# Kernel optimization log

Hardware: AMD Instinct MI355X
Metric: run time of the kernel (lower is better)

## Reference

```python
import jax, jax.numpy as jnp
import numpy as np

B, S, H = 4, 8192, 768
NH, HD = 12, 64          # num_heads, head_size
M = 64                   # projection_dim = min(256, HD)
EPS = 1e-6

def setup_inputs() -> dict:
    key = jax.random.key(0)
    ks = jax.random.split(key, 10)
    scale_w = 0.02
    scale_p = 1.0 / np.sqrt(HD)
    return {
        'hidden_states': jax.random.normal(ks[0], (B, S, H), jnp.float32),
        'Wq': jax.random.normal(ks[1], (H, H), jnp.float32) * scale_w,
        'bq': jnp.zeros((H,), jnp.float32),
        'Wk': jax.random.normal(ks[2], (H, H), jnp.float32) * scale_w,
        'bk': jnp.zeros((H,), jnp.float32),
        'Wv': jax.random.normal(ks[3], (H, H), jnp.float32) * scale_w,
        'bv': jnp.zeros((H,), jnp.float32),
        'Wo': jax.random.normal(ks[4], (H, H), jnp.float32) * scale_w,
        'bo': jnp.zeros((H,), jnp.float32),
        'projection_matrix': jax.random.normal(ks[5], (NH, HD, M), jnp.float32) * scale_p,
    }

def reference(hidden_states, Wq, bq, Wk, bk, Wv, bv, Wo, bo, projection_matrix):
    b, s, h = hidden_states.shape
    def heads(x):  # [b,s,h] -> [b,nh,s,hd]
        return x.reshape(b, s, NH, HD).transpose(0, 2, 1, 3)
    q = heads(hidden_states @ Wq + bq)
    k = heads(hidden_states @ Wk + bk)
    v = heads(hidden_states @ Wv + bv)
    # random-feature projection + stabilized exp feature map
    qp = jnp.einsum('bhnd,hdm->bhnm', q, projection_matrix)
    kp = jnp.einsum('bhnd,hdm->bhnm', k, projection_matrix)
    qp = jnp.exp(qp - jnp.max(qp, axis=-1, keepdims=True))
    kp = jnp.exp(kp - jnp.max(kp, axis=-1, keepdims=True))
    # O(n) linear attention: kv summary [b,h,m,hd]
    kv = jnp.einsum('bhnm,bhnd->bhmd', kp, v)
    qkv = jnp.einsum('bhnm,bhmd->bhnd', qp, kv)
    k_sum = jnp.sum(kp, axis=2)                      # [b,h,m]
    normalizer = jnp.einsum('bhnm,bhm->bhn', qp, k_sum)[..., None]
    ctx = qkv / (normalizer + EPS)
    ctx = ctx.transpose(0, 2, 1, 3).reshape(b, s, NH * HD)
    return ctx @ Wo + bo
```

## Files before the change

### kernel.cpp

```cpp
#include <hip/hip_runtime.h>
#include <hip/hip_bf16.h>


#define S_    8192
#define H_    768
#define NH_   12
#define EPS_  1e-6f

typedef unsigned short U16;
typedef short bf16x8 __attribute__((ext_vector_type(8)));
typedef float f32x4  __attribute__((ext_vector_type(4)));

__device__ __forceinline__ U16 f2b(float x) {
  unsigned u = __float_as_uint(x);
  return (U16)((u + 0x7fffu + ((u >> 16) & 1u)) >> 16);
}
__device__ __forceinline__ float b2f(U16 h) {
  return __uint_as_float(((unsigned)h) << 16);
}
__device__ __forceinline__ void gl2lds16(const void* g, void* l) {
  __builtin_amdgcn_global_load_lds(
      (const __attribute__((address_space(1))) void*)g,
      (__attribute__((address_space(3))) void*)l, 16, 0, 0);
}

__global__ __launch_bounds__(256) void prologue(
    const float* __restrict__ hs, const float* __restrict__ Wq,
    const float* __restrict__ bq, const float* __restrict__ Wk,
    const float* __restrict__ bk, const float* __restrict__ Wv,
    const float* __restrict__ bv, const float* __restrict__ Wo,
    const float* __restrict__ P,
    U16* __restrict__ hs_hi, U16* __restrict__ WcatH, U16* __restrict__ WoTH,
    float* __restrict__ biasC, float* __restrict__ zbase) {
  __shared__ float sm[8192];
  const int bid = blockIdx.x, tid = threadIdx.x;
  if (bid < 960) {
    zbase[bid * 256 + tid] = 0.f;
    return;
  }
  if (bid < 25536) {
    int i = (bid - 960) * 256 + tid;
    float4 x = ((const float4*)hs)[i];
    ushort4 h;
    h.x = f2b(x.x); h.y = f2b(x.y); h.z = f2b(x.z); h.w = f2b(x.w);
    ((ushort4*)hs_hi)[i] = h;
    return;
  }
  if (bid < 25824) {
    int f = bid - 25536;
    int z = f / 144, rem = f - z * 144, h = rem / 12, kcB = rem - (rem / 12) * 12;
    float* Pl = sm;
    float* WL = sm + 4096;
    const float* W = z ? Wk : Wq;
    const float4* P4 = (const float4*)(P + (size_t)h * 4096);
#pragma unroll
    for (int p = 0; p < 4; ++p) ((float4*)Pl)[tid + p * 256] = P4[tid + p * 256];
#pragma unroll
    for (int p = 0; p < 4; ++p) {
      int idx = tid + p * 256;
      int kk = idx >> 4, d4 = (idx & 15) * 4;
      *(float4*)&WL[kk * 64 + d4] =
          *(const float4*)&W[(size_t)(kcB * 64 + kk) * H_ + h * 64 + d4];
    }
    __syncthreads();
    const int m = tid & 63, kg = tid >> 6;
    float acc[16] = {};
    for (int d = 0; d < 64; ++d) {
      float pv = Pl[d * 64 + m];
#pragma unroll
      for (int k2 = 0; k2 < 16; ++k2) acc[k2] += WL[(kg * 16 + k2) * 64 + d] * pv;
    }
    U16* dst = WcatH + (size_t)(z * 768 + h * 64 + m) * H_ + kcB * 64 + kg * 16;
#pragma unroll
    for (int k2 = 0; k2 < 16; k2 += 4) {
      ushort4 o;
      o.x = f2b(acc[k2]); o.y = f2b(acc[k2 + 1]);
      o.z = f2b(acc[k2 + 2]); o.w = f2b(acc[k2 + 3]);
      *(ushort4*)&dst[k2] = o;
    }
    if (kcB == 0 && tid < 64) {
      const float* bb = z ? bk : bq;
      float a2 = 0.f;
      for (int d = 0; d < 64; ++d) a2 += bb[h * 64 + d] * Pl[d * 64 + tid];
      biasC[z * 768 + h * 64 + tid] = a2;
    }
    return;
  }
  const int isWo = bid >= 25968;
  int v = bid - (isWo ? 25968 : 25824);
  int kb = v / 12, rb = v - kb * 12;
  const float* W = isWo ? Wo : Wv;
  float (*T)[68] = (float(*)[68])sm;
#pragma unroll
  for (int p = 0; p < 4; ++p) {
    int idx = tid + p * 256;
    int rr = idx >> 4, c4 = (idx & 15) * 4;
    float4 x = *(const float4*)&W[(size_t)(kb * 64 + rr) * H_ + rb * 64 + c4];
    T[rr][c4] = x.x; T[rr][c4 + 1] = x.y; T[rr][c4 + 2] = x.z; T[rr][c4 + 3] = x.w;
  }
  __syncthreads();
  U16* dst = isWo ? WoTH : WcatH;
  const int rbase = (isWo ? 0 : 1536) + rb * 64;
#pragma unroll
  for (int p = 0; p < 4; ++p) {
    int idx = tid + p * 256;
    int r2 = idx >> 4, c2 = (idx & 15) * 4;
    ushort4 o;
    o.x = f2b(T[c2 + 0][r2]); o.y = f2b(T[c2 + 1][r2]);
    o.z = f2b(T[c2 + 2][r2]); o.w = f2b(T[c2 + 3][r2]);
    *(ushort4*)&dst[(size_t)(rbase + r2) * H_ + kb * 64 + c2] = o;
  }
  if (!isWo && kb == 0 && rb == 0) {
#pragma unroll
    for (int p = 0; p < 3; ++p) biasC[1536 + tid + p * 256] = bv[tid + p * 256];
  }
}

__global__ __launch_bounds__(256, 2) void gemm_qkv(
    const U16* __restrict__ Ahi, const U16* __restrict__ Bhi,
    const float* __restrict__ bias,
    U16* __restrict__ qp, U16* __restrict__ kpT, U16* __restrict__ vT) {
  __shared__ __align__(16) U16 Us[32768];
  const int tid = threadIdx.x, w = tid >> 6, lane = tid & 63;
  const int quad = lane >> 4, l16 = lane & 15;
  const int b = blockIdx.x;
  const int mt = b & 255, nt0 = b >> 8;
  const int rowA0 = mt * 128;
  const int wm = w & 1, wn = w >> 1;
  const U16* srcA[4];
  int rowBl[4];
  unsigned ldsc[4];
  const int kch = ((lane & 7) ^ (lane >> 3)) * 8;
#pragma unroll
  for (int t = 0; t < 4; ++t) {
    int c = w * 4 + t;
    int row = c * 8 + (lane >> 3);
    srcA[t] = Ahi + (size_t)(rowA0 + row) * H_ + kch;
    rowBl[t] = row;
    ldsc[t] = (unsigned)c * 512;
  }
  auto stage = [&](int jn, int tn, int bi) {
    const int colB = (nt0 + 2 * jn) * 128;
    unsigned ub = (unsigned)bi * 16384u;
#pragma unroll
    for (int t = 0; t < 4; ++t) {
      gl2lds16(srcA[t] + tn * 64, &Us[ub + ldsc[t]]);
      gl2lds16(Bhi + (size_t)(colB + rowBl[t]) * H_ + tn * 64 + kch,
               &Us[ub + 8192u + ldsc[t]]);
    }
  };

  stage(0, 0, 0);
  for (int jj = 0; jj < 9; ++jj) {
    const int colB0 = (nt0 + 2 * jj) * 128;
    f32x4 acc[4][4] = {};
    for (int t = 0; t < 12; ++t) {
      const bool more = !(jj == 8 && t == 11);
      if (more) {
        if (t < 11) stage(jj, t + 1, (t + 1) & 1);
        else        stage(jj + 1, 0, 0);
        asm volatile("s_waitcnt vmcnt(8)" ::: "memory");
      } else {
        asm volatile("s_waitcnt vmcnt(0)" ::: "memory");
      }
      __builtin_amdgcn_sched_barrier(0);
      __builtin_amdgcn_s_barrier();
      __builtin_amdgcn_sched_barrier(0);
      const unsigned ab = (unsigned)(t & 1) * 16384u;
      bf16x8 ah[4][2], bh[4][2];
#pragma unroll
      for (int i = 0; i < 4; ++i)
#pragma unroll
        for (int ks = 0; ks < 2; ++ks)
          ah[i][ks] = *(const bf16x8*)&Us[ab +
              (unsigned)((wm * 64 + i * 16 + l16) * 64 +
                         (((ks * 4 + quad) ^ (l16 & 7)) * 8))];
#pragma unroll
      for (int j = 0; j < 4; ++j)
#pragma unroll
        for (int ks = 0; ks < 2; ++ks)
          bh[j][ks] = *(const bf16x8*)&Us[ab + 8192u +
              (unsigned)((wn * 64 + j * 16 + l16) * 64 +
                         (((ks * 4 + quad) ^ (l16 & 7)) * 8))];
      asm volatile("s_waitcnt lgkmcnt(0)" ::: "memory");
      __builtin_amdgcn_sched_barrier(0);
      __builtin_amdgcn_s_setprio(1);
#pragma unroll
      for (int ks = 0; ks < 2; ++ks)
#pragma unroll
        for (int j = 0; j < 4; ++j)
#pragma unroll
          for (int i = 0; i < 4; ++i)
            acc[i][j] = __builtin_amdgcn_mfma_f32_16x16x32_bf16(
                ah[i][ks], bh[j][ks], acc[i][j], 0, 0, 0);
      __builtin_amdgcn_s_setprio(0);
      __builtin_amdgcn_sched_barrier(0);
      __builtin_amdgcn_s_barrier();
      __builtin_amdgcn_sched_barrier(0);
    }
    const int col64 = colB0 + wn * 64;
    float bj[4];
#pragma unroll
    for (int j = 0; j < 4; ++j) bj[j] = bias[col64 + j * 16 + l16];
    if (col64 < 768) {
      const int h = col64 >> 6;
#pragma unroll
      for (int i = 0; i < 4; ++i) {
#pragma unroll
        for (int r = 0; r < 4; ++r) {
          int row = rowA0 + wm * 64 + i * 16 + quad * 4 + r;
          float v0 = acc[i][0][r] + bj[0], v1 = acc[i][1][r] + bj[1];
          float v2 = acc[i][2][r] + bj[2], v3 = acc[i][3][r] + bj[3];
          float mx = fmaxf(fmaxf(v0, v1), fmaxf(v2, v3));
          mx = fmaxf(mx, __shfl_xor(mx, 1));
          mx = fmaxf(mx, __shfl_xor(mx, 2));
          mx = fmaxf(mx, __shfl_xor(mx, 4));
          mx = fmaxf(mx, __shfl_xor(mx, 8));
          int bb = row >> 13, s = row & 8191;
          size_t base = ((size_t)(bb * NH_ + h) * S_ + s) * 64 + l16;
          qp[base +  0] = f2b(__expf(v0 - mx));
          qp[base + 16] = f2b(__expf(v1 - mx));
          qp[base + 32] = f2b(__expf(v2 - mx));
          qp[base + 48] = f2b(__expf(v3 - mx));
        }
      }
    } else {
      const int isv = col64 >= 1536;
      const int h = (col64 - (isv ? 1536 : 768)) >> 6;
      U16* dstT = isv ? vT : kpT;
      const int bh2 = (rowA0 >> 13) * NH_ + h;
#pragma unroll
      for (int i = 0; i < 4; ++i) {
        float er[4][4];
#pragma unroll
        for (int r = 0; r < 4; ++r) {
          float v0 = acc[i][0][r] + bj[0], v1 = acc[i][1][r] + bj[1];
          float v2 = acc[i][2][r] + bj[2], v3 = acc[i][3][r] + bj[3];
          if (!isv) {
            float mx = fmaxf(fmaxf(v0, v1), fmaxf(v2, v3));
            mx = fmaxf(mx, __shfl_xor(mx, 1));
            mx = fmaxf(mx, __shfl_xor(mx, 2));
            mx = fmaxf(mx, __shfl_xor(mx, 4));
            mx = fmaxf(mx, __shfl_xor(mx, 8));
            v0 = __expf(v0 - mx); v1 = __expf(v1 - mx);
            v2 = __expf(v2 - mx); v3 = __expf(v3 - mx);
          }
          er[0][r] = v0; er[1][r] = v1; er[2][r] = v2; er[3][r] = v3;
        }
        int n = rowA0 + wm * 64 + i * 16 + quad * 4;
        int s = n & 8191;
#pragma unroll
        for (int j = 0; j < 4; ++j) {
          ushort4 o;
          o.x = f2b(er[j][0]); o.y = f2b(er[j][1]);
          o.z = f2b(er[j][2]); o.w = f2b(er[j][3]);
          *(ushort4*)&dstT[((size_t)bh2 * 64 + j * 16 + l16) * S_ + s] = o;
        }
      }
    }
  }
}

__global__ __launch_bounds__(256, 4) void kv_accum_mfma(
    const U16* __restrict__ kpT, const U16* __restrict__ vT,
    float* __restrict__ kvT) {
  __shared__ __align__(16) U16 Us[2 * 64 * 64];
  const int tid = threadIdx.x, w = tid >> 6, lane = tid & 63;
  const int quad = lane >> 4, l16 = lane & 15;
  const int bh = blockIdx.y;
  const int n0 = blockIdx.x * 512;
  const U16* srcs[4];
  unsigned ldsoff[4];
#pragma unroll
  for (int t = 0; t < 4; ++t) {
    int c = w * 4 + t, buf = c >> 3;
    int r = (c & 7) * 8 + (lane >> 3);
    const U16* base = buf ? kpT : vT;
    srcs[t] = base + ((size_t)bh * 64 + r) * S_ + n0 + (lane & 7) * 8;
    ldsoff[t] = buf * 4096 + (c & 7) * 512;
  }
  f32x4 acc[4] = {};
  float ks[4] = {0.f, 0.f, 0.f, 0.f};
  for (int nc = 0; nc < 512; nc += 64) {
#pragma unroll
    for (int t = 0; t < 4; ++t) gl2lds16(srcs[t] + nc, &Us[ldsoff[t]]);
    __syncthreads();
#pragma unroll
    for (int k0 = 0; k0 < 64; k0 += 32) {
      bf16x8 av = *(const bf16x8*)&Us[(w * 16 + l16) * 64 + k0 + quad * 8];
#pragma unroll
      for (int j = 0; j < 4; ++j) {
        bf16x8 bk = *(const bf16x8*)&Us[4096 + (j * 16 + l16) * 64 + k0 + quad * 8];
        if (w == 0) {
#pragma unroll
          for (int e = 0; e < 8; ++e) ks[j] += b2f((U16)bk[e]);
        }
        acc[j] = __builtin_amdgcn_mfma_f32_16x16x32_bf16(av, bk, acc[j], 0, 0, 0);
      }
    }
    __syncthreads();
  }
#pragma unroll
  for (int j = 0; j < 4; ++j)
#pragma unroll
    for (int r = 0; r < 4; ++r) {
      int d = w * 16 + quad * 4 + r;
      atomicAdd(&kvT[((size_t)bh * 80 + d) * 64 + j * 16 + l16], acc[j][r]);
    }
  if (w == 0) {
#pragma unroll
    for (int j = 0; j < 4; ++j) {
      ks[j] += __shfl_xor(ks[j], 16);
      ks[j] += __shfl_xor(ks[j], 32);
    }
    if (lane < 16) {
#pragma unroll
      for (int j = 0; j < 4; ++j)
        atomicAdd(&kvT[((size_t)bh * 80 + 64) * 64 + j * 16 + lane], ks[j]);
    }
  }
}

__global__ __launch_bounds__(256) void ctx_gemm_k(
    const U16* __restrict__ qp, const float* __restrict__ kvT,
    U16* __restrict__ ctx) {
  __shared__ __align__(16) U16 As[128 * 64];
  __shared__ __align__(16) U16 Bs[80 * 64];
  int bh = blockIdx.y, row0 = blockIdx.x * 128;
  int tid = threadIdx.x, w = tid >> 6, lane = tid & 63;
  int quad = lane >> 4, l16 = lane & 15;
  const U16* Ab = qp + ((size_t)bh * S_ + row0) * 64;
#pragma unroll
  for (int t = 0; t < 4; ++t) {
    int cb = (w * 4 + t) * 64;
    gl2lds16(Ab + (size_t)(cb + lane) * 8, &As[cb * 8]);
  }
  const float4* kv4 = (const float4*)(kvT + (size_t)bh * 5120);
#pragma unroll
  for (int t = 0; t < 5; ++t) {
    int idx = t * 256 + tid;
    float4 f = kv4[idx];
    ushort4 o;
    o.x = f2b(f.x); o.y = f2b(f.y); o.z = f2b(f.z); o.w = f2b(f.w);
    *(ushort4*)&Bs[idx * 4] = o;
  }
  __syncthreads();
  f32x4 acc[2][5] = {};
#pragma unroll
  for (int k0 = 0; k0 < 64; k0 += 32) {
    bf16x8 a[2], fb[5];
#pragma unroll
    for (int i = 0; i < 2; ++i)
      a[i] = *(const bf16x8*)&As[(w * 32 + i * 16 + l16) * 64 + k0 + quad * 8];
#pragma unroll
    for (int j = 0; j < 5; ++j)
      fb[j] = *(const bf16x8*)&Bs[(j * 16 + l16) * 64 + k0 + quad * 8];
#pragma unroll
    for (int j = 0; j < 5; ++j)
#pragma unroll
      for (int i = 0; i < 2; ++i)
        acc[i][j] = __builtin_amdgcn_mfma_f32_16x16x32_bf16(a[i], fb[j], acc[i][j], 0, 0, 0);
  }
  int b = bh / NH_, h = bh - b * NH_;
#pragma unroll
  for (int i = 0; i < 2; ++i) {
#pragma unroll
    for (int r = 0; r < 4; ++r) {
      int s = row0 + w * 32 + i * 16 + quad * 4 + r;
      float nv = __shfl(acc[i][4][r], lane & 48);
      float inv = 1.f / (nv + EPS_);
      size_t base = ((size_t)b * S_ + s) * H_ + h * 64;
#pragma unroll
      for (int j = 0; j < 4; ++j)
        ctx[base + j * 16 + l16] = f2b(acc[i][j][r] * inv);
    }
  }
}

__global__ __launch_bounds__(256, 2) void out_gemm(
    const U16* __restrict__ Ahi, const U16* __restrict__ Bhi,
    const float* __restrict__ bias, float* __restrict__ C) {
  __shared__ __align__(16) U16 Us[32768];
  const int tid = threadIdx.x, w = tid >> 6, lane = tid & 63;
  const int quad = lane >> 4, l16 = lane & 15;
  const int b = blockIdx.x;
  const int mt = b & 255, nt0 = b >> 8;
  const int rowA0 = mt * 128;
  const int wm = w & 1, wn = w >> 1;
  const U16* srcA[4];
  int rowBl[4];
  unsigned ldsc[4];
  const int kch = ((lane & 7) ^ (lane >> 3)) * 8;
#pragma unroll
  for (int t = 0; t < 4; ++t) {
    int c = w * 4 + t;
    int row = c * 8 + (lane >> 3);
    srcA[t] = Ahi + (size_t)(rowA0 + row) * H_ + kch;
    rowBl[t] = row;
    ldsc[t] = (unsigned)c * 512;
  }
  auto stage = [&](int jn, int tn, int bi) {
    const int colB = (nt0 + 2 * jn) * 128;
    unsigned ub = (unsigned)bi * 16384u;
#pragma unroll
    for (int t = 0; t < 4; ++t) {
      gl2lds16(srcA[t] + tn * 64, &Us[ub + ldsc[t]]);
      gl2lds16(Bhi + (size_t)(colB + rowBl[t]) * H_ + tn * 64 + kch,
               &Us[ub + 8192u + ldsc[t]]);
    }
  };

  stage(0, 0, 0);
  for (int jj = 0; jj < 3; ++jj) {
    const int colB0 = (nt0 + 2 * jj) * 128;
    f32x4 acc[4][4] = {};
    for (int t = 0; t < 12; ++t) {
      const bool more = !(jj == 2 && t == 11);
      if (more) {
        if (t < 11) stage(jj, t + 1, (t + 1) & 1);
        else        stage(jj + 1, 0, 0);
        asm volatile("s_waitcnt vmcnt(8)" ::: "memory");
      } else {
        asm volatile("s_waitcnt vmcnt(0)" ::: "memory");
      }
      __builtin_amdgcn_sched_barrier(0);
      __builtin_amdgcn_s_barrier();
      __builtin_amdgcn_sched_barrier(0);
      const unsigned ab = (unsigned)(t & 1) * 16384u;
      bf16x8 ah[4][2], bh[4][2];
#pragma unroll
      for (int i = 0; i < 4; ++i)
#pragma unroll
        for (int ks = 0; ks < 2; ++ks)
          ah[i][ks] = *(const bf16x8*)&Us[ab +
              (unsigned)((wm * 64 + i * 16 + l16) * 64 +
                         (((ks * 4 + quad) ^ (l16 & 7)) * 8))];
#pragma unroll
      for (int j = 0; j < 4; ++j)
#pragma unroll
        for (int ks = 0; ks < 2; ++ks)
          bh[j][ks] = *(const bf16x8*)&Us[ab + 8192u +
              (unsigned)((wn * 64 + j * 16 + l16) * 64 +
                         (((ks * 4 + quad) ^ (l16 & 7)) * 8))];
      asm volatile("s_waitcnt lgkmcnt(0)" ::: "memory");
      __builtin_amdgcn_sched_barrier(0);
      __builtin_amdgcn_s_setprio(1);
#pragma unroll
      for (int ks = 0; ks < 2; ++ks)
#pragma unroll
        for (int j = 0; j < 4; ++j)
#pragma unroll
          for (int i = 0; i < 4; ++i)
            acc[i][j] = __builtin_amdgcn_mfma_f32_16x16x32_bf16(
                ah[i][ks], bh[j][ks], acc[i][j], 0, 0, 0);
      __builtin_amdgcn_s_setprio(0);
      __builtin_amdgcn_sched_barrier(0);
      __builtin_amdgcn_s_barrier();
      __builtin_amdgcn_sched_barrier(0);
    }
#pragma unroll
    for (int i = 0; i < 4; ++i) {
      int row = rowA0 + wm * 64 + i * 16 + quad * 4;
#pragma unroll
      for (int j = 0; j < 4; ++j) {
        int col = colB0 + wn * 64 + j * 16 + l16;
        float bvv = bias[col];
#pragma unroll
        for (int r = 0; r < 4; ++r)
          C[(size_t)(row + r) * H_ + col] = acc[i][j][r] + bvv;
      }
    }
  }
}

extern "C" void kernel_launch(void* const* d_in, const int* in_sizes, int n_in,
                              void* d_out, int out_size, void* d_ws, size_t ws_size,
                              hipStream_t stream) {
  const float* hs = (const float*)d_in[0];
  const float* Wq = (const float*)d_in[1];
  const float* bq = (const float*)d_in[2];
  const float* Wk = (const float*)d_in[3];
  const float* bk = (const float*)d_in[4];
  const float* Wv = (const float*)d_in[5];
  const float* bv = (const float*)d_in[6];
  const float* Wo = (const float*)d_in[7];
  const float* bo = (const float*)d_in[8];
  const float* P  = (const float*)d_in[9];
  float* out = (float*)d_out;

  char* ws = (char*)d_ws;
  size_t off = 0;
  auto alloc = [&](size_t bytes) -> void* {
    void* p = ws + off;
    off = (off + bytes + 255) & ~(size_t)255;
    return p;
  };
  U16*   hs_hi = (U16*)alloc(50331648);
  U16*   WcatH = (U16*)alloc(3538944);
  U16*   WoTH  = (U16*)alloc(1179648);
  float* biasC = (float*)alloc(9216);
  U16*   qp    = (U16*)alloc(50331648);
  U16*   kpT   = (U16*)alloc(50331648);
  U16*   vT    = (U16*)alloc(50331648);
  float* kvT   = (float*)alloc(983040);
  U16*   ctx   = hs_hi;

  prologue<<<dim3(26112), dim3(256), 0, stream>>>(
      hs, Wq, bq, Wk, bk, Wv, bv, Wo, P, hs_hi, WcatH, WoTH, biasC, kvT);
  gemm_qkv<<<dim3(512), dim3(256), 0, stream>>>(hs_hi, WcatH, biasC, qp, kpT, vT);
  kv_accum_mfma<<<dim3(16, 48), dim3(256), 0, stream>>>(kpT, vT, kvT);
  ctx_gemm_k<<<dim3(64, 48), dim3(256), 0, stream>>>(qp, kvT, ctx);
  out_gemm<<<dim3(512), dim3(256), 0, stream>>>(ctx, WoTH, bo, out);
}
```

Baseline: 461.5 us.

## Halve QKV GEMM block to two waves with 128x64 per-wave tiles; spread k_sum across waves

The fused QKV GEMM now launches 128-thread blocks (2 waves). Each wave computes a 128x64 output tile in two 64-row halves that reuse the same B fragments, so each wave issues twice as many global-to-LDS loads per stage. The aim is more MFMA work per wave and fewer B fragment reads from LDS. The cost is twice the accumulator registers per wave and fewer waves available to hide latency. In the kv accumulation kernel, the k_sum reduction is split so each wave sums one 16-column slice, instead of wave 0 doing all four.

```diff
diff --git a/kernel.cpp b/kernel.cpp
--- a/kernel.cpp
+++ b/kernel.cpp
@@ -116,7 +116,7 @@
   }
 }
 
-__global__ __launch_bounds__(256, 2) void gemm_qkv(
+__global__ __launch_bounds__(128, 2) void gemm_qkv(
     const U16* __restrict__ Ahi, const U16* __restrict__ Bhi,
     const float* __restrict__ bias,
     U16* __restrict__ qp, U16* __restrict__ kpT, U16* __restrict__ vT) {
@@ -126,40 +126,33 @@
   const int b = blockIdx.x;
   const int mt = b & 255, nt0 = b >> 8;
   const int rowA0 = mt * 128;
-  const int wm = w & 1, wn = w >> 1;
-  const U16* srcA[4];
-  int rowBl[4];
-  unsigned ldsc[4];
   const int kch = ((lane & 7) ^ (lane >> 3)) * 8;
-#pragma unroll
-  for (int t = 0; t < 4; ++t) {
-    int c = w * 4 + t;
-    int row = c * 8 + (lane >> 3);
-    srcA[t] = Ahi + (size_t)(rowA0 + row) * H_ + kch;
-    rowBl[t] = row;
-    ldsc[t] = (unsigned)c * 512;
-  }
+  const U16* a0 = Ahi + (size_t)(rowA0 + w * 64 + (lane >> 3)) * H_ + kch;
+  const U16* b0 = Bhi + (size_t)(w * 64 + (lane >> 3)) * H_ + kch;
+  const unsigned lds0 = (unsigned)(w * 8) * 512u;
+
   auto stage = [&](int jn, int tn, int bi) {
-    const int colB = (nt0 + 2 * jn) * 128;
-    unsigned ub = (unsigned)bi * 16384u;
-#pragma unroll
-    for (int t = 0; t < 4; ++t) {
-      gl2lds16(srcA[t] + tn * 64, &Us[ub + ldsc[t]]);
-      gl2lds16(Bhi + (size_t)(colB + rowBl[t]) * H_ + tn * 64 + kch,
-               &Us[ub + 8192u + ldsc[t]]);
+    const size_t colOff = (size_t)((nt0 + 2 * jn) * 128) * H_;
+    unsigned ub = (unsigned)bi * 16384u + lds0;
+    const U16* ap = a0 + tn * 64;
+    const U16* bp = b0 + colOff + tn * 64;
+#pragma unroll
+    for (int t = 0; t < 8; ++t) {
+      gl2lds16(ap + t * (8 * H_), &Us[ub + t * 512u]);
+      gl2lds16(bp + t * (8 * H_), &Us[ub + 8192u + t * 512u]);
     }
   };
 
   stage(0, 0, 0);
   for (int jj = 0; jj < 9; ++jj) {
     const int colB0 = (nt0 + 2 * jj) * 128;
-    f32x4 acc[4][4] = {};
+    f32x4 acc[8][4] = {};
     for (int t = 0; t < 12; ++t) {
       const bool more = !(jj == 8 && t == 11);
       if (more) {
         if (t < 11) stage(jj, t + 1, (t + 1) & 1);
         else        stage(jj + 1, 0, 0);
-        asm volatile("s_waitcnt vmcnt(8)" ::: "memory");
+        asm volatile("s_waitcnt vmcnt(16)" ::: "memory");
       } else {
         asm volatile("s_waitcnt vmcnt(0)" ::: "memory");
       }
@@ -169,18 +162,18 @@
       const unsigned ab = (unsigned)(t & 1) * 16384u;
       bf16x8 ah[4][2], bh[4][2];
 #pragma unroll
+      for (int j = 0; j < 4; ++j)
+#pragma unroll
+        for (int ks = 0; ks < 2; ++ks)
+          bh[j][ks] = *(const bf16x8*)&Us[ab + 8192u +
+              (unsigned)((w * 64 + j * 16 + l16) * 64 +
+                         (((ks * 4 + quad) ^ (l16 & 7)) * 8))];
+#pragma unroll
       for (int i = 0; i < 4; ++i)
 #pragma unroll
         for (int ks = 0; ks < 2; ++ks)
           ah[i][ks] = *(const bf16x8*)&Us[ab +
-              (unsigned)((wm * 64 + i * 16 + l16) * 64 +
-                         (((ks * 4 + quad) ^ (l16 & 7)) * 8))];
-#pragma unroll
-      for (int j = 0; j < 4; ++j)
-#pragma unroll
-        for (int ks = 0; ks < 2; ++ks)
-          bh[j][ks] = *(const bf16x8*)&Us[ab + 8192u +
-              (unsigned)((wn * 64 + j * 16 + l16) * 64 +
+              (unsigned)((i * 16 + l16) * 64 +
                          (((ks * 4 + quad) ^ (l16 & 7)) * 8))];
       asm volatile("s_waitcnt lgkmcnt(0)" ::: "memory");
       __builtin_amdgcn_sched_barrier(0);
@@ -194,21 +187,40 @@
             acc[i][j] = __builtin_amdgcn_mfma_f32_16x16x32_bf16(
                 ah[i][ks], bh[j][ks], acc[i][j], 0, 0, 0);
       __builtin_amdgcn_s_setprio(0);
+#pragma unroll
+      for (int i = 0; i < 4; ++i)
+#pragma unroll
+        for (int ks = 0; ks < 2; ++ks)
+          ah[i][ks] = *(const bf16x8*)&Us[ab +
+              (unsigned)(((64 + i * 16) + l16) * 64 +
+                         (((ks * 4 + quad) ^ (l16 & 7)) * 8))];
+      asm volatile("s_waitcnt lgkmcnt(0)" ::: "memory");
+      __builtin_amdgcn_sched_barrier(0);
+      __builtin_amdgcn_s_setprio(1);
+#pragma unroll
+      for (int ks = 0; ks < 2; ++ks)
+#pragma unroll
+        for (int j = 0; j < 4; ++j)
+#pragma unroll
+          for (int i = 0; i < 4; ++i)
+            acc[4 + i][j] = __builtin_amdgcn_mfma_f32_16x16x32_bf16(
+                ah[i][ks], bh[j][ks], acc[4 + i][j], 0, 0, 0);
+      __builtin_amdgcn_s_setprio(0);
       __builtin_amdgcn_sched_barrier(0);
       __builtin_amdgcn_s_barrier();
       __builtin_amdgcn_sched_barrier(0);
     }
-    const int col64 = colB0 + wn * 64;
+    const int col64 = colB0 + w * 64;
     float bj[4];
 #pragma unroll
     for (int j = 0; j < 4; ++j) bj[j] = bias[col64 + j * 16 + l16];
     if (col64 < 768) {
       const int h = col64 >> 6;
 #pragma unroll
-      for (int i = 0; i < 4; ++i) {
+      for (int i = 0; i < 8; ++i) {
 #pragma unroll
         for (int r = 0; r < 4; ++r) {
-          int row = rowA0 + wm * 64 + i * 16 + quad * 4 + r;
+          int row = rowA0 + i * 16 + quad * 4 + r;
           float v0 = acc[i][0][r] + bj[0], v1 = acc[i][1][r] + bj[1];
           float v2 = acc[i][2][r] + bj[2], v3 = acc[i][3][r] + bj[3];
           float mx = fmaxf(fmaxf(v0, v1), fmaxf(v2, v3));
@@ -230,7 +242,7 @@
       U16* dstT = isv ? vT : kpT;
       const int bh2 = (rowA0 >> 13) * NH_ + h;
 #pragma unroll
-      for (int i = 0; i < 4; ++i) {
+      for (int i = 0; i < 8; ++i) {
         float er[4][4];
 #pragma unroll
         for (int r = 0; r < 4; ++r) {
@@ -247,7 +259,7 @@
           }
           er[0][r] = v0; er[1][r] = v1; er[2][r] = v2; er[3][r] = v3;
         }
-        int n = rowA0 + wm * 64 + i * 16 + quad * 4;
+        int n = rowA0 + i * 16 + quad * 4;
         int s = n & 8191;
 #pragma unroll
         for (int j = 0; j < 4; ++j) {
@@ -280,7 +292,7 @@
     ldsoff[t] = buf * 4096 + (c & 7) * 512;
   }
   f32x4 acc[4] = {};
-  float ks[4] = {0.f, 0.f, 0.f, 0.f};
+  float kss = 0.f;
   for (int nc = 0; nc < 512; nc += 64) {
 #pragma unroll
     for (int t = 0; t < 4; ++t) gl2lds16(srcs[t] + nc, &Us[ldsoff[t]]);
@@ -291,9 +303,9 @@
 #pragma unroll
       for (int j = 0; j < 4; ++j) {
         bf16x8 bk = *(const bf16x8*)&Us[4096 + (j * 16 + l16) * 64 + k0 + quad * 8];
-        if (w == 0) {
-#pragma unroll
-          for (int e = 0; e < 8; ++e) ks[j] += b2f((U16)bk[e]);
+        if (j == w) {
+#pragma unroll
+          for (int e = 0; e < 8; ++e) kss += b2f((U16)bk[e]);
         }
         acc[j] = __builtin_amdgcn_mfma_f32_16x16x32_bf16(av, bk, acc[j], 0, 0, 0);
       }
@@ -307,18 +319,10 @@
       int d = w * 16 + quad * 4 + r;
       atomicAdd(&kvT[((size_t)bh * 80 + d) * 64 + j * 16 + l16], acc[j][r]);
     }
-  if (w == 0) {
-#pragma unroll
-    for (int j = 0; j < 4; ++j) {
-      ks[j] += __shfl_xor(ks[j], 16);
-      ks[j] += __shfl_xor(ks[j], 32);
-    }
-    if (lane < 16) {
-#pragma unroll
-      for (int j = 0; j < 4; ++j)
-        atomicAdd(&kvT[((size_t)bh * 80 + 64) * 64 + j * 16 + lane], ks[j]);
-    }
-  }
+  kss += __shfl_xor(kss, 16);
+  kss += __shfl_xor(kss, 32);
+  if (lane < 16)
+    atomicAdd(&kvT[((size_t)bh * 80 + 64) * 64 + w * 16 + lane], kss);
 }
 
 __global__ __launch_bounds__(256) void ctx_gemm_k(
@@ -507,7 +511,7 @@
 
   prologue<<<dim3(26112), dim3(256), 0, stream>>>(
       hs, Wq, bq, Wk, bk, Wv, bv, Wo, P, hs_hi, WcatH, WoTH, biasC, kvT);
-  gemm_qkv<<<dim3(512), dim3(256), 0, stream>>>(hs_hi, WcatH, biasC, qp, kpT, vT);
+  gemm_qkv<<<dim3(512), dim3(128), 0, stream>>>(hs_hi, WcatH, biasC, qp, kpT, vT);
   kv_accum_mfma<<<dim3(16, 48), dim3(256), 0, stream>>>(kpT, vT, kvT);
   ctx_gemm_k<<<dim3(64, 48), dim3(256), 0, stream>>>(qp, kvT, ctx);
   out_gemm<<<dim3(512), dim3(256), 0, stream>>>(ctx, WoTH, bo, out);
```

Result: slower. 535.4 us (+16.0%).
